# Kernel optimization log

Hardware: AMD Instinct MI355X
Metric: run time of the kernel (lower is better)

Reference implementation:

```python
import jax, jax.numpy as jnp
import numpy as np

N_AGENTS, RNN_H, N_HEADS, GAT_D, EMB, SDIM = 16, 64, 4, 32, 32, 128


def setup_inputs() -> dict:
    key = jax.random.key(0)
    ks = jax.random.split(key, 16)
    xav = lambda k, shp: jax.random.normal(k, shp, jnp.float32) * (2.0 / sum(shp)) ** 0.5
    return {
        'agent_qs': jax.random.normal(ks[0], (32, 128, N_AGENTS), jnp.float32),
        'states': jax.random.normal(ks[1], (32, 128, SDIM), jnp.float32),
        'hidden_states': jax.random.normal(ks[2], (32, 128, N_AGENTS, RNN_H), jnp.float32),
        'uncertainty': jax.random.uniform(ks[3], (32, 128, 1), jnp.float32),
        'W_gat': xav(ks[4], (RNN_H, N_HEADS * GAT_D)) * 1.414,
        'att_a': xav(ks[5], (1, N_HEADS, 2 * GAT_D)) * 1.414,
        'w1s_W': xav(ks[6], (SDIM + 1, N_HEADS * EMB * GAT_D)),
        'w1s_b': jnp.zeros((N_HEADS * EMB * GAT_D,), jnp.float32),
        'b1_W': xav(ks[7], (SDIM, EMB)),
        'b1_b': jnp.zeros((EMB,), jnp.float32),
        'wf_W': xav(ks[8], (SDIM, EMB)),
        'wf_b': jnp.zeros((EMB,), jnp.float32),
        'V1_W': xav(ks[9], (SDIM, EMB)),
        'V1_b': jnp.zeros((EMB,), jnp.float32),
        'V2_W': xav(ks[10], (EMB, 1)),
        'V2_b': jnp.zeros((1,), jnp.float32),
    }


def gat(h, W_gat, att_a):
    B, n, _ = h.shape
    hp = (h @ W_gat).reshape(B, n, N_HEADS, GAT_D).transpose(0, 2, 1, 3)  # (B,H,n,d)
    a_src, a_dst = att_a[0, :, :GAT_D], att_a[0, :, GAT_D:]  # (H,d) each
    # e[b,h,i,j] = <hp_i, a_src> + <hp_j, a_dst>  (same math as concat+dot)
    src = jnp.einsum('bhnd,hd->bhn', hp, a_src)
    dst = jnp.einsum('bhnd,hd->bhn', hp, a_dst)
    e = jax.nn.leaky_relu(src[:, :, :, None] + dst[:, :, None, :], 0.2)
    attn = jax.nn.softmax(e, axis=-1)
    return jax.nn.elu(jnp.einsum('bhij,bhjd->bhid', attn, hp))  # (B,H,n,d)


def reference(agent_qs, states, hidden_states, uncertainty, W_gat, att_a,
              w1s_W, w1s_b, b1_W, b1_b, wf_W, wf_b, V1_W, V1_b, V2_W, V2_b):
    bs = agent_qs.shape[0]
    s = states.reshape(-1, SDIM)                      # (B,S)
    qs = agent_qs.reshape(-1, 1, N_AGENTS)            # (B,1,n)
    hs = hidden_states.reshape(-1, N_AGENTS, RNN_H)   # (B,n,R)
    unc = uncertainty.reshape(-1, 1)
    s_aug = jnp.concatenate([s, unc], axis=1)         # (B,S+1)

    g = gat(hs, W_gat, att_a)                         # (B,H,n,d)

    w1_state = (s_aug @ w1s_W + w1s_b).reshape(-1, N_HEADS, EMB, GAT_D)
    w1_heads = jnp.abs(jnp.einsum('bhed,bhnd->bhen', w1_state, g))  # (B,H,E,n)
    w1 = w1_heads.mean(axis=1).transpose(0, 2, 1)     # (B,n,E)

    b1 = (s @ b1_W + b1_b)[:, None, :]                # (B,1,E)
    hidden = jax.nn.elu(jnp.einsum('bin,bne->bie', qs, w1) + b1)  # (B,1,E)

    w_final = jnp.abs(s @ wf_W + wf_b)[:, :, None]    # (B,E,1)
    v = (jax.nn.relu(s @ V1_W + V1_b) @ V2_W + V2_b)[:, None, :]  # (B,1,1)
    y = jnp.einsum('bie,bej->bij', hidden, w_final) + v
    return y.reshape(bs, -1, 1)
```

## Files before the change

### kernel.cpp

```cpp
#include <hip/hip_runtime.h>
#include <hip/hip_bf16.h>
#include <math.h>


typedef __attribute__((ext_vector_type(8))) short short8;
typedef __attribute__((ext_vector_type(8))) unsigned short ushort8;
typedef __attribute__((ext_vector_type(4))) float float4v;
typedef __attribute__((ext_vector_type(4))) _Float16 half4v;

static __device__ inline unsigned short f2bf(float f) {
    unsigned int x;
    __builtin_memcpy(&x, &f, 4);
    unsigned int r = x + 0x7fffu + ((x >> 16) & 1u);
    return (unsigned short)(r >> 16);
}

static __device__ inline unsigned int cvtpk(float lo, float hi) {
    __hip_bfloat162 h = __float22bfloat162_rn(make_float2(lo, hi));
    unsigned int u;
    __builtin_memcpy(&u, &h, 4);
    return u;
}

static __device__ inline short8 pack8(float4 f0, float4 f1) {
    unsigned int u[4] = {cvtpk(f0.x, f0.y), cvtpk(f0.z, f0.w),
                         cvtpk(f1.x, f1.y), cvtpk(f1.z, f1.w)};
    short8 s;
    __builtin_memcpy(&s, u, 16);
    return s;
}

__global__ __launch_bounds__(256) void kA_fused(
    const float* __restrict__ w1s_W,
    const float* __restrict__ W_gat,
    const float* __restrict__ att_a,
    const float* __restrict__ states,
    const float* __restrict__ uncertainty,
    const float* __restrict__ w1s_b,
    const float* __restrict__ b1_W, const float* __restrict__ b1_b,
    const float* __restrict__ wf_W, const float* __restrict__ wf_b,
    const float* __restrict__ V1_W, const float* __restrict__ V1_b,
    const float* __restrict__ V2_W, const float* __restrict__ V2_b,
    unsigned short* __restrict__ WgTf,
    unsigned short* __restrict__ W2,
    float* __restrict__ b1v, float* __restrict__ wfv,
    float* __restrict__ out)
{
    __shared__ __align__(16) unsigned short T[128 * 72];
    const int tid = threadIdx.x, bx = blockIdx.x;
    const int wave = tid >> 6, lane = tid & 63;
    const int m = lane & 15, quad = lane >> 4;

    if (bx < 64) {
        const int b0w = bx * 64 + wave * 16;

        short8 a[4];
        #pragma unroll
        for (int ks = 0; ks < 4; ++ks) {
            const float* sp = states + (size_t)(b0w + m) * 128 + ks * 32 + quad * 8;
            a[ks] = pack8(*(const float4*)sp, *(const float4*)(sp + 4));
        }
        float4v accT[6];
        #pragma unroll
        for (int nt = 0; nt < 6; ++nt) accT[nt] = (float4v){0.f, 0.f, 0.f, 0.f};
        #pragma unroll
        for (int nt = 0; nt < 6; ++nt) {
            const float* Wset = (nt < 2) ? b1_W : (nt < 4 ? wf_W : V1_W);
            const int e = (nt & 1) * 16 + m;
            #pragma unroll
            for (int ks = 0; ks < 4; ++ks) {
                unsigned int u[4];
                #pragma unroll
                for (int jp = 0; jp < 4; ++jp) {
                    float g0 = Wset[(ks * 32 + quad * 8 + 2 * jp) * 32 + e];
                    float g1 = Wset[(ks * 32 + quad * 8 + 2 * jp + 1) * 32 + e];
                    u[jp] = cvtpk(g0, g1);
                }
                short8 bf;
                __builtin_memcpy(&bf, u, 16);
                accT[nt] = __builtin_amdgcn_mfma_f32_16x16x32_bf16(a[ks], bf, accT[nt], 0, 0, 0);
            }
        }
        float vsum[4] = {0.f, 0.f, 0.f, 0.f};
        #pragma unroll
        for (int p = 0; p < 2; ++p) {
            const int e = p * 16 + m;
            const float bb1 = b1_b[e], bwf = wf_b[e], bv1 = V1_b[e], v2 = V2_W[e];
            #pragma unroll
            for (int reg = 0; reg < 4; ++reg) {
                const int row = b0w + quad * 4 + reg;
                b1v[(size_t)row * 32 + e] = accT[p][reg] + bb1;
                wfv[(size_t)row * 32 + e] = fabsf(accT[2 + p][reg] + bwf);
                vsum[reg] += fmaxf(accT[4 + p][reg] + bv1, 0.f) * v2;
            }
        }
        #pragma unroll
        for (int reg = 0; reg < 4; ++reg) {
            vsum[reg] += __shfl_xor(vsum[reg], 1);
            vsum[reg] += __shfl_xor(vsum[reg], 2);
            vsum[reg] += __shfl_xor(vsum[reg], 4);
            vsum[reg] += __shfl_xor(vsum[reg], 8);
        }
        if (m == 0) {
            #pragma unroll
            for (int reg = 0; reg < 4; ++reg)
                out[b0w + quad * 4 + reg] = vsum[reg] + V2_b[0];
        }
    } else if (bx == 64) {
        #pragma unroll
        for (int t = 0; t < 32; ++t) {
            int i = t * 256 + tid;
            int k = i >> 7, c = i & 127;
            T[c * 72 + k] = f2bf(W_gat[k * 128 + c]);
        }
        __syncthreads();
        #pragma unroll
        for (int t = 0; t < 4; ++t) {
            int i = t * 256 + tid;
            int nt = i >> 7, w = i & 127;
            int kh = w >> 6, q = (w >> 4) & 3, mm = w & 15;
            *(ushort8*)&WgTf[nt * 1024 + w * 8] =
                *(const ushort8*)&T[(nt * 16 + mm) * 72 + kh * 32 + q * 8];
        }
        {
            const int k = tid >> 2, h = tid & 3;
            float ss = 0.f, dd = 0.f;
            #pragma unroll
            for (int d = 0; d < 32; ++d) {
                float wv = W_gat[k * 128 + h * 32 + d];
                ss = fmaf(wv, att_a[h * 64 + d], ss);
                dd = fmaf(wv, att_a[h * 64 + 32 + d], dd);
            }
            const int base = 8192 + (k >> 5) * 512 + ((k >> 3) & 3) * 128 + (k & 7);
            WgTf[base + h * 8]       = f2bf(ss);
            WgTf[base + (4 + h) * 8] = f2bf(dd);
        }
        #pragma unroll
        for (int t = 0; t < 2; ++t) {
            int i = t * 256 + tid;
            int kh = i >> 8, q2 = (i >> 6) & 3, mm = 8 + ((i >> 3) & 7), j = i & 7;
            WgTf[8192 + kh * 512 + q2 * 128 + mm * 8 + j] = 0;
        }
    } else {
        const int gb = bx - 65;
        const int rb = gb >> 5, pg = gb & 31;
        const int E = pg * 4 + wave;
        const int ct0 = E * 2;

        const float* w128 = w1s_W + (size_t)128 * 4096;

        short8 A[2][4];
        #pragma unroll
        for (int t = 0; t < 2; ++t) {
            const int col = (ct0 + t) * 16 + m;
            #pragma unroll
            for (int ks = 0; ks < 4; ++ks) {
                unsigned int u[4];
                #pragma unroll
                for (int jp = 0; jp < 4; ++jp) {
                    float g0 = w1s_W[(size_t)(ks * 32 + quad * 8 + 2 * jp) * 4096 + col];
                    float g1 = w1s_W[(size_t)(ks * 32 + quad * 8 + 2 * jp + 1) * 4096 + col];
                    u[jp] = cvtpk(g0, g1);
                }
                __builtin_memcpy(&A[t][ks], u, 16);
            }
        }

        float wf[2][4], bb[2][4];
        #pragma unroll
        for (int t = 0; t < 2; ++t) {
            float4 w4 = *(const float4*)&w128[(ct0 + t) * 16 + quad * 4];
            float4 b4 = *(const float4*)&w1s_b[(ct0 + t) * 16 + quad * 4];
            wf[t][0] = w4.x; wf[t][1] = w4.y; wf[t][2] = w4.z; wf[t][3] = w4.w;
            bb[t][0] = b4.x; bb[t][1] = b4.y; bb[t][2] = b4.z; bb[t][3] = b4.w;
        }

        const int eo = (E >> 4) * 512 + (E & 15) * 32 + quad * 8;

        #pragma unroll
        for (int c = 0; c < 4; ++c) {
            const int r0c = rb * 64 + c * 16;
            const float us = uncertainty[r0c + m];
            short8 Bf[4];
            #pragma unroll
            for (int ks = 0; ks < 4; ++ks) {
                const float* sp = states + (size_t)(r0c + m) * 128 + ks * 32 + quad * 8;
                Bf[ks] = pack8(*(const float4*)sp, *(const float4*)(sp + 4));
            }

            float4v z0 = (float4v){0.f, 0.f, 0.f, 0.f};
            float4v z1 = (float4v){0.f, 0.f, 0.f, 0.f};
            #pragma unroll
            for (int ks = 0; ks < 4; ++ks) {
                z0 = __builtin_amdgcn_mfma_f32_16x16x32_bf16(A[0][ks], Bf[ks], z0, 0, 0, 0);
                z1 = __builtin_amdgcn_mfma_f32_16x16x32_bf16(A[1][ks], Bf[ks], z1, 0, 0, 0);
            }
            unsigned int wpk[4];
            #pragma unroll
            for (int reg = 0; reg < 4; ++reg) {
                float za = z0[reg] + us * wf[0][reg] + bb[0][reg];
                float zb = z1[reg] + us * wf[1][reg] + bb[1][reg];
                wpk[reg] = cvtpk(za, zb);
            }
            short8 pk;
            __builtin_memcpy(&pk, wpk, 16);
            *(short8*)&W2[(size_t)(r0c + m) * 4096 + eo] = pk;
        }
    }
}

__global__ __launch_bounds__(256) void k1_gatmix(
    const float* __restrict__ hidden_states,
    const unsigned short* __restrict__ WgTf,
    const unsigned short* __restrict__ W2,
    const float* __restrict__ agent_qs,
    const float* __restrict__ b1v, const float* __restrict__ wfv,
    float* __restrict__ out)
{
    const int wave = threadIdx.x >> 6;
    const int b = blockIdx.x * 4 + wave;
    const int lane = threadIdx.x & 63, m = lane & 15, quad = lane >> 4;
    __shared__ __align__(16) float sc[4 * 320];
    float* scr = &sc[wave * 320];

    short8 wfr[8];
    #pragma unroll
    for (int i = 0; i < 8; ++i)
        wfr[i] = *(const short8*)&W2[(size_t)b * 4096 + i * 512 + m * 32 + quad * 8];
    const float qs_m = agent_qs[b * 16 + m];

    const float* hrow = hidden_states + ((size_t)b * 16 + m) * 64;
    float4 f0 = *(const float4*)(hrow + quad * 8);
    float4 f1 = *(const float4*)(hrow + quad * 8 + 4);
    short8 a0 = pack8(f0, f1);
    f0 = *(const float4*)(hrow + 32 + quad * 8);
    f1 = *(const float4*)(hrow + 32 + quad * 8 + 4);
    short8 a1 = pack8(f0, f1);

    float4v hpt[9];
    #pragma unroll
    for (int nt = 0; nt < 9; ++nt) {
        short8 bf0 = *(const short8*)&WgTf[nt * 1024 + lane * 8];
        short8 bf1 = *(const short8*)&WgTf[nt * 1024 + 512 + lane * 8];
        float4v z = (float4v){0.f, 0.f, 0.f, 0.f};
        z = __builtin_amdgcn_mfma_f32_16x16x32_bf16(a0, bf0, z, 0, 0, 0);
        z = __builtin_amdgcn_mfma_f32_16x16x32_bf16(a1, bf1, z, 0, 0, 0);
        hpt[nt] = z;
    }

    {
        float4 pr = {hpt[8][0], hpt[8][1], hpt[8][2], hpt[8][3]};
        *(float4*)&scr[m * 20 + quad * 4] = pr;
    }

    float Sacc[2][4] = {};

    #pragma unroll
    for (int h = 0; h < 4; ++h) {
        const float src_m = scr[h * 20 + m];
        float4 pdv = *(const float4*)&scr[(4 + h) * 20 + quad * 4];
        float pd[4] = {pdv.x, pdv.y, pdv.z, pdv.w};

        float e_[4];
        #pragma unroll
        for (int jj = 0; jj < 4; ++jj) {
            float x = src_m + pd[jj];
            e_[jj] = fmaxf(x, 0.2f * x);
        }
        float mx = fmaxf(fmaxf(e_[0], e_[1]), fmaxf(e_[2], e_[3]));
        mx = fmaxf(mx, __shfl_xor(mx, 16));
        mx = fmaxf(mx, __shfl_xor(mx, 32));
        float p_[4], ssum = 0.f;
        #pragma unroll
        for (int jj = 0; jj < 4; ++jj) { p_[jj] = __expf(e_[jj] - mx); ssum += p_[jj]; }
        ssum += __shfl_xor(ssum, 16);
        ssum += __shfl_xor(ssum, 32);
        const float inv = __builtin_amdgcn_rcpf(ssum);

        half4v bfrag;
        #pragma unroll
        for (int jj = 0; jj < 4; ++jj) bfrag[jj] = (_Float16)(p_[jj] * inv);

        float4v zp[2];
        #pragma unroll
        for (int p = 0; p < 2; ++p) {
            float4v ct = hpt[2 * h + p];
            half4v afrag;
            #pragma unroll
            for (int t = 0; t < 4; ++t) afrag[t] = (_Float16)ct[t];
            float4v z = (float4v){0.f, 0.f, 0.f, 0.f};
            zp[p] = __builtin_amdgcn_mfma_f32_16x16x16f16(afrag, bfrag, z, 0, 0, 0);
        }
        unsigned int w[4];
        #pragma unroll
        for (int t = 0; t < 4; ++t) {
            float x0 = zp[0][t];
            x0 = (x0 > 0.f) ? x0 : (__expf(x0) - 1.f);
            float x1 = zp[1][t];
            x1 = (x1 > 0.f) ? x1 : (__expf(x1) - 1.f);
            w[t] = cvtpk(x0, x1);
        }
        short8 gfrag;
        __builtin_memcpy(&gfrag, w, 16);

        #pragma unroll
        for (int H = 0; H < 2; ++H) {
            float4v z = (float4v){0.f, 0.f, 0.f, 0.f};
            z = __builtin_amdgcn_mfma_f32_16x16x32_bf16(wfr[h * 2 + H], gfrag, z, 0, 0, 0);
            #pragma unroll
            for (int reg = 0; reg < 4; ++reg)
                Sacc[H][reg] += fabsf(z[reg]);
        }
    }

    float local = 0.f;
    #pragma unroll
    for (int H = 0; H < 2; ++H) {
        float sn[4];
        #pragma unroll
        for (int reg = 0; reg < 4; ++reg) sn[reg] = Sacc[H][reg] * qs_m;
        #pragma unroll
        for (int mask = 1; mask <= 8; mask <<= 1) {
            #pragma unroll
            for (int reg = 0; reg < 4; ++reg) sn[reg] += __shfl_xor(sn[reg], mask);
        }
        float4 b4 = *(const float4*)&b1v[(size_t)b * 32 + H * 16 + quad * 4];
        float4 w4 = *(const float4*)&wfv[(size_t)b * 32 + H * 16 + quad * 4];
        float bq[4] = {b4.x, b4.y, b4.z, b4.w};
        float wq[4] = {w4.x, w4.y, w4.z, w4.w};
        #pragma unroll
        for (int reg = 0; reg < 4; ++reg) {
            float hid = 0.25f * sn[reg] + bq[reg];
            hid = (hid > 0.f) ? hid : expm1f(hid);
            local = fmaf(hid, wq[reg], local);
        }
    }
    local += __shfl_xor(local, 16);
    local += __shfl_xor(local, 32);
    if (lane == 0) out[b] = out[b] + local;
}

extern "C" void kernel_launch(void* const* d_in, const int* in_sizes, int n_in,
                              void* d_out, int out_size, void* d_ws, size_t ws_size,
                              hipStream_t stream)
{
    const float* agent_qs      = (const float*)d_in[0];
    const float* states        = (const float*)d_in[1];
    const float* hidden_states = (const float*)d_in[2];
    const float* uncertainty   = (const float*)d_in[3];
    const float* W_gat         = (const float*)d_in[4];
    const float* att_a         = (const float*)d_in[5];
    const float* w1s_W         = (const float*)d_in[6];
    const float* w1s_b         = (const float*)d_in[7];
    const float* b1_W          = (const float*)d_in[8];
    const float* b1_b          = (const float*)d_in[9];
    const float* wf_W          = (const float*)d_in[10];
    const float* wf_b          = (const float*)d_in[11];
    const float* V1_W          = (const float*)d_in[12];
    const float* V1_b          = (const float*)d_in[13];
    const float* V2_W          = (const float*)d_in[14];
    const float* V2_b          = (const float*)d_in[15];

    char* w = (char*)d_ws;
    unsigned short* WgTf    = (unsigned short*)w;  w += (size_t)9216 * 2;
    unsigned short* W2      = (unsigned short*)w;  w += (size_t)16777216 * 2;
    float* b1v              = (float*)w;           w += (size_t)131072 * 4;
    float* wfv              = (float*)w;           w += (size_t)131072 * 4;
    float* out              = (float*)d_out;

    kA_fused<<<2113, 256, 0, stream>>>(w1s_W, W_gat, att_a, states, uncertainty,
                                       w1s_b, b1_W, b1_b, wf_W, wf_b,
                                       V1_W, V1_b, V2_W, V2_b,
                                       WgTf, W2, b1v, wfv, out);

    k1_gatmix<<<1024, 256, 0, stream>>>(hidden_states, WgTf, W2, agent_qs,
                                        b1v, wfv, out);
}
```

Before: 143.1 us.

## Pre-pack w1s_W into bf16 MFMA fragment layout and raise MFMA wave priority

Adds a small pre-pass kernel that converts w1s_W to bf16 once and stores it in the exact fragment order the W2-producing blocks load. Those blocks then read each fragment with one 16-byte load instead of strided scalar fp32 loads that every row-block repeated. The mix kernel also wraps its MFMA sections in s_setprio to favour waves issuing matrix work. This costs an extra kernel launch and a 1 MB workspace buffer.

```diff
diff --git a/kernel.cpp b/kernel.cpp
--- a/kernel.cpp
+++ b/kernel.cpp
@@ -30,13 +30,33 @@
     return s;
 }
 
-__global__ __launch_bounds__(256) void kA_fused(
+__global__ __launch_bounds__(256) void k0_pack(
+    const float* __restrict__ w1s_W,
+    unsigned short* __restrict__ w1sTf)
+{
+    __shared__ __align__(16) unsigned short T[16 * 136];
+    const int tid = threadIdx.x, bx = blockIdx.x;
+    const int c0 = bx * 16;
+    const int cc = tid & 15, kr = tid >> 4;
+    #pragma unroll
+    for (int t = 0; t < 8; ++t) {
+        int k = t * 16 + kr;
+        T[cc * 136 + k] = f2bf(w1s_W[(size_t)k * 4096 + c0 + cc]);
+    }
+    __syncthreads();
+    const int ks = tid >> 6, q = (tid >> 4) & 3, mm = tid & 15;
+    *(ushort8*)&w1sTf[(size_t)bx * 2048 + tid * 8] =
+        *(const ushort8*)&T[mm * 136 + ks * 32 + q * 8];
+}
+
+__global__ __launch_bounds__(256) void kB_fused(
     const float* __restrict__ w1s_W,
     const float* __restrict__ W_gat,
     const float* __restrict__ att_a,
     const float* __restrict__ states,
     const float* __restrict__ uncertainty,
     const float* __restrict__ w1s_b,
+    const unsigned short* __restrict__ w1sTf,
     const float* __restrict__ b1_W, const float* __restrict__ b1_b,
     const float* __restrict__ wf_W, const float* __restrict__ wf_b,
     const float* __restrict__ V1_W, const float* __restrict__ V1_b,
@@ -151,20 +171,10 @@
 
         short8 A[2][4];
         #pragma unroll
-        for (int t = 0; t < 2; ++t) {
-            const int col = (ct0 + t) * 16 + m;
-            #pragma unroll
-            for (int ks = 0; ks < 4; ++ks) {
-                unsigned int u[4];
-                #pragma unroll
-                for (int jp = 0; jp < 4; ++jp) {
-                    float g0 = w1s_W[(size_t)(ks * 32 + quad * 8 + 2 * jp) * 4096 + col];
-                    float g1 = w1s_W[(size_t)(ks * 32 + quad * 8 + 2 * jp + 1) * 4096 + col];
-                    u[jp] = cvtpk(g0, g1);
-                }
-                __builtin_memcpy(&A[t][ks], u, 16);
-            }
-        }
+        for (int t = 0; t < 2; ++t)
+            #pragma unroll
+            for (int ks = 0; ks < 4; ++ks)
+                A[t][ks] = *(const short8*)&w1sTf[(size_t)(ct0 + t) * 2048 + ks * 512 + lane * 8];
 
         float wf[2][4], bb[2][4];
         #pragma unroll
@@ -238,6 +248,7 @@
     short8 a1 = pack8(f0, f1);
 
     float4v hpt[9];
+    __builtin_amdgcn_s_setprio(1);
     #pragma unroll
     for (int nt = 0; nt < 9; ++nt) {
         short8 bf0 = *(const short8*)&WgTf[nt * 1024 + lane * 8];
@@ -247,6 +258,7 @@
         z = __builtin_amdgcn_mfma_f32_16x16x32_bf16(a1, bf1, z, 0, 0, 0);
         hpt[nt] = z;
     }
+    __builtin_amdgcn_s_setprio(0);
 
     {
         float4 pr = {hpt[8][0], hpt[8][1], hpt[8][2], hpt[8][3]};
@@ -282,6 +294,7 @@
         for (int jj = 0; jj < 4; ++jj) bfrag[jj] = (_Float16)(p_[jj] * inv);
 
         float4v zp[2];
+        __builtin_amdgcn_s_setprio(1);
         #pragma unroll
         for (int p = 0; p < 2; ++p) {
             float4v ct = hpt[2 * h + p];
@@ -291,6 +304,7 @@
             float4v z = (float4v){0.f, 0.f, 0.f, 0.f};
             zp[p] = __builtin_amdgcn_mfma_f32_16x16x16f16(afrag, bfrag, z, 0, 0, 0);
         }
+        __builtin_amdgcn_s_setprio(0);
         unsigned int w[4];
         #pragma unroll
         for (int t = 0; t < 4; ++t) {
@@ -303,6 +317,7 @@
         short8 gfrag;
         __builtin_memcpy(&gfrag, w, 16);
 
+        __builtin_amdgcn_s_setprio(1);
         #pragma unroll
         for (int H = 0; H < 2; ++H) {
             float4v z = (float4v){0.f, 0.f, 0.f, 0.f};
@@ -311,6 +326,7 @@
             for (int reg = 0; reg < 4; ++reg)
                 Sacc[H][reg] += fabsf(z[reg]);
         }
+        __builtin_amdgcn_s_setprio(0);
     }
 
     float local = 0.f;
@@ -362,14 +378,17 @@
     const float* V2_b          = (const float*)d_in[15];
 
     char* w = (char*)d_ws;
+    unsigned short* w1sTf   = (unsigned short*)w;  w += (size_t)524288 * 2;
     unsigned short* WgTf    = (unsigned short*)w;  w += (size_t)9216 * 2;
     unsigned short* W2      = (unsigned short*)w;  w += (size_t)16777216 * 2;
     float* b1v              = (float*)w;           w += (size_t)131072 * 4;
     float* wfv              = (float*)w;           w += (size_t)131072 * 4;
     float* out              = (float*)d_out;
 
-    kA_fused<<<2113, 256, 0, stream>>>(w1s_W, W_gat, att_a, states, uncertainty,
-                                       w1s_b, b1_W, b1_b, wf_W, wf_b,
+    k0_pack<<<256, 256, 0, stream>>>(w1s_W, w1sTf);
+
+    kB_fused<<<2113, 256, 0, stream>>>(w1s_W, W_gat, att_a, states, uncertainty,
+                                       w1s_b, w1sTf, b1_W, b1_b, wf_W, wf_b,
                                        V1_W, V1_b, V2_W, V2_b,
                                        WgTf, W2, b1v, wfv, out);
 
```

New measurement: 149.9 us. +4.7%, slower.
